# Optimization experiments

Measured on AMD Instinct MI355X. Metric: run time of the kernel, lower is better.

The kernel has to match this reference:

```python
import jax, jax.numpy as jnp
import numpy as np

N = 100_000      # nodes
E = 1_600_000    # edges (before self loops)
F_IN = 128       # dataset.num_node_features
H = 64           # hidden_channels
C = 10           # dataset.num_classes
B = 128          # graphs in batch
NEG_SLOPE = 0.2  # GATConv default


def setup_inputs() -> dict:
    key = jax.random.key(0)
    ks = jax.random.split(key, 16)
    s = 0.05
    x = jax.random.normal(ks[0], (N, F_IN), jnp.float32)
    edge_index = jax.random.randint(ks[1], (2, E), 0, N, dtype=jnp.int32).astype(jnp.int64)
    batch = jnp.sort(jax.random.randint(ks[2], (N,), 0, B, dtype=jnp.int32)).astype(jnp.int64)
    inp = {"x": x, "edge_index": edge_index, "batch": batch}
    # GATConv params: lin weight [out,in], att_src/att_dst [out], bias [out]
    dims = [(H, F_IN), (H, H), (H, H)]
    for i, (o, fi) in enumerate(dims, start=1):
        k = jax.random.split(ks[2 + i], 4)
        inp[f"W{i}"] = jax.random.normal(k[0], (o, fi), jnp.float32) * s
        inp[f"a_src{i}"] = jax.random.normal(k[1], (o,), jnp.float32) * s
        inp[f"a_dst{i}"] = jax.random.normal(k[2], (o,), jnp.float32) * s
        inp[f"b{i}"] = jax.random.normal(k[3], (o,), jnp.float32) * s
    inp["W_lin"] = jax.random.normal(ks[8], (C, H), jnp.float32) * s
    inp["b_lin"] = jax.random.normal(ks[9], (C,), jnp.float32) * s
    return inp


def gat_conv(x, src, dst, W, a_src, a_dst, b):
    # x: [N,Fin]; src/dst: [E+N] (self loops appended)
    h = x @ W.T                      # [N,H]
    e_src = h @ a_src                # [N] per-node src score
    e_dst = h @ a_dst                # [N] per-node dst score
    e = jax.nn.leaky_relu(e_src[src] + e_dst[dst], NEG_SLOPE)  # [E+N]
    # segment softmax over incoming edges of each dst node
    m = jax.ops.segment_max(e, dst, num_segments=N)
    ex = jnp.exp(e - m[dst])
    denom = jax.ops.segment_sum(ex, dst, num_segments=N)
    alpha = ex / denom[dst]          # [E+N]
    out = jax.ops.segment_sum(h[src] * alpha[:, None], dst, num_segments=N)
    return out + b


def reference(x, edge_index, batch, W1, a_src1, a_dst1, b1,
              W2, a_src2, a_dst2, b2, W3, a_src3, a_dst3, b3,
              W_lin, b_lin):
    loops = jnp.arange(N, dtype=edge_index.dtype)
    src = jnp.concatenate([edge_index[0], loops])
    dst = jnp.concatenate([edge_index[1], loops])
    h = jax.nn.relu(gat_conv(x, src, dst, W1, a_src1, a_dst1, b1))
    h = jax.nn.relu(gat_conv(h, src, dst, W2, a_src2, a_dst2, b2))
    h = gat_conv(h, src, dst, W3, a_src3, a_dst3, b3)
    # global mean pool over graphs
    sums = jax.ops.segment_sum(h, batch, num_segments=B)          # [B,H]
    cnt = jax.ops.segment_sum(jnp.ones((N,), h.dtype), batch, num_segments=B)
    pooled = sums / jnp.maximum(cnt, 1.0)[:, None]
    # dropout is identity in eval mode
    return pooled @ W_lin.T + b_lin   # [B,C]
```

## Files before the change

kernel.cpp:

```cpp
#include <hip/hip_runtime.h>
#include <hip/hip_bf16.h>

#define NN 100000
#define EE 1600000
#define ETOT 1700000
#define FIN1 128
#define HD 64
#define NC 10
#define NB 128
#define NEG 0.2f
#define LOG2E 1.44269504f

#define NBKT 196
#define BCAP 10240
#define BLKE 4096
#define ABLOCKS ((ETOT + BLKE - 1) / BLKE)
#define GBLOCKS ((NN + 63) / 64)


static constexpr size_t OFF_HA   = 0;
static constexpr size_t OFF_HB   = (size_t)NN * HD;
static constexpr size_t OFF_ESA  = (size_t)NN * HD * 2;
static constexpr size_t OFF_EDA  = OFF_ESA + (size_t)NN * 4;
static constexpr size_t OFF_ESB  = OFF_EDA + (size_t)NN * 4;
static constexpr size_t OFF_EDB  = OFF_ESB + (size_t)NN * 4;
static constexpr size_t OFF_ROW  = OFF_EDB + (size_t)NN * 4;
static constexpr size_t OFF_CSR  = OFF_ROW + (size_t)(NN + 4) * 4;
static constexpr size_t OFF_GC   = OFF_CSR + (size_t)ETOT * 4;
static constexpr size_t OFF_POOL = OFF_GC + 1024;
static constexpr size_t OFF_BKT  = OFF_POOL + (size_t)NB * HD * 4;

typedef __attribute__((ext_vector_type(8))) short short8;
typedef __attribute__((ext_vector_type(4))) float floatx4;
typedef __attribute__((ext_vector_type(2))) float floatx2;

__device__ __forceinline__ unsigned short f2bf(float f) {
  unsigned u = __float_as_uint(f);
  if ((u & 0x7F800000u) == 0x7F800000u) return (unsigned short)(u >> 16);
  return (unsigned short)((u + 0x7FFFu + ((u >> 16) & 1u)) >> 16);
}
__device__ __forceinline__ unsigned pk2(float a, float b) {
  return (unsigned)f2bf(a) | ((unsigned)f2bf(b) << 16);
}

#if __has_builtin(__builtin_amdgcn_cvt_pk_fp8_f32) && __has_builtin(__builtin_amdgcn_cvt_pk_f32_fp8)
#define HW_FP8 1
#endif
__device__ __forceinline__ unsigned enc1_fp8(float f) {
  _Float16 hf = (_Float16)f;
  unsigned short b = __builtin_bit_cast(unsigned short, hf);
  unsigned s = ((unsigned)b >> 8) & 0x80u;
  int mag = b & 0x7fff;
  if (mag < 0x2380) return s;
  int r = mag + 0x3F + ((mag >> 7) & 1);
  int m = (r >> 7) - 64;
  if (m > 0x7E) m = 0x7E;
  return s | (unsigned)m;
}
__device__ __forceinline__ unsigned pack4_fp8(float a, float b, float c, float d) {
#ifdef HW_FP8
  int w = __builtin_amdgcn_cvt_pk_fp8_f32(a, b, 0, false);
  w = __builtin_amdgcn_cvt_pk_fp8_f32(c, d, w, true);
  return (unsigned)w;
#else
  return enc1_fp8(a) | (enc1_fp8(b) << 8) | (enc1_fp8(c) << 16) | (enc1_fp8(d) << 24);
#endif
}
__device__ __forceinline__ float dec1_fp8(unsigned byte) {
  unsigned short hb = (unsigned short)(((byte & 0x80u) << 8) | ((byte & 0x7fu) << 7));
  _Float16 hf = __builtin_bit_cast(_Float16, hb);
  return (float)hf * 256.0f;
}
template <bool HI>
__device__ __forceinline__ floatx2 unpk2_fp8(unsigned w) {
#ifdef HW_FP8
  return __builtin_amdgcn_cvt_pk_f32_fp8((int)w, HI);
#else
  unsigned s = HI ? (w >> 16) : w;
  floatx2 r; r.x = dec1_fp8(s & 0xffu); r.y = dec1_fp8((s >> 8) & 0xffu);
  return r;
#endif
}

__device__ __forceinline__ void bucketA_body(
    int bid, const int* __restrict__ EI, unsigned* __restrict__ bucketed,
    int* __restrict__ gcur, char* smem) {
  unsigned* stage = (unsigned*)smem;
  unsigned short* sb = (unsigned short*)(smem + BLKE * 4);
  int* cnt  = (int*)(smem + BLKE * 4 + BLKE * 2);
  int* lofs = cnt + NBKT;
  int* base = lofs + NBKT;
  int* sc   = base + NBKT;
  const int t = threadIdx.x;
  const long long start = (long long)bid * BLKE;
  long long rem = (long long)ETOT - start;
  const int V = (rem < BLKE) ? (int)rem : BLKE;
  unsigned pk[BLKE / 256];
  short bk[BLKE / 256];
  for (int i = t; i < NBKT; i += 256) cnt[i] = 0;
  __syncthreads();
#pragma unroll
  for (int j = 0; j < BLKE / 256; j++) {
    long long k = start + t + 256 * j;
    bk[j] = -1;
    if (k < ETOT) {
      int s, d;
      if (k < EE) { s = EI[k]; d = EI[(long long)EE + k]; }
      else        { s = d = (int)(k - EE); }
      int b = d >> 9;
      pk[j] = ((unsigned)s << 9) | (unsigned)(d & 511);
      bk[j] = (short)b;
      atomicAdd(&cnt[b], 1);
    }
  }
  __syncthreads();
  int own = (t < NBKT) ? cnt[t] : 0;
  sc[t] = own;
  __syncthreads();
  for (int off = 1; off < 256; off <<= 1) {
    int add = (t >= off) ? sc[t - off] : 0;
    __syncthreads();
    sc[t] += add;
    __syncthreads();
  }
  if (t < NBKT) {
    lofs[t] = sc[t] - own;
    base[t] = (own > 0) ? atomicAdd(&gcur[t], own) : 0;
    cnt[t] = 0;
  }
  __syncthreads();
#pragma unroll
  for (int j = 0; j < BLKE / 256; j++) {
    if (bk[j] >= 0) {
      int b = bk[j];
      int p = lofs[b] + atomicAdd(&cnt[b], 1);
      stage[p] = pk[j];
      sb[p] = (unsigned short)b;
    }
  }
  __syncthreads();
  for (int i = t; i < V; i += 256) {
    int b = sb[i];
    int pos = base[b] + (i - lofs[b]);
    if (pos < BCAP) bucketed[(long long)b * BCAP + pos] = stage[i];
  }
}

__device__ __forceinline__ void gemm1_body(
    int bid, const float* __restrict__ X, const float* __restrict__ W,
    const float* __restrict__ As, const float* __restrict__ Ad,
    unsigned* __restrict__ hout, float* __restrict__ es, float* __restrict__ ed,
    char* smem) {
  constexpr int K = FIN1, RW = K / 2;
  unsigned* Xw = (unsigned*)smem;
  unsigned* Ww = (unsigned*)(smem + 16384);
  const int t = threadIdx.x;
  const int nodeBase = bid * 64;

  for (int i4 = t * 4; i4 < 64 * K; i4 += 1024) {
    int node = i4 >> 7, k = i4 & (K - 1);
    float4 v = make_float4(0.f, 0.f, 0.f, 0.f);
    if (nodeBase + node < NN)
      v = *(const float4*)(X + ((long long)(nodeBase + node) << 7) + k);
    uint2 p = make_uint2(pk2(v.x, v.y), pk2(v.z, v.w));
    int kw = k >> 1;
    *(uint2*)&Xw[node * RW + (kw ^ ((node & 7) << 2))] = p;
  }
  for (int i4 = t * 4; i4 < 64 * K; i4 += 1024) {
    int f = i4 >> 7, k = i4 & (K - 1);
    float4 v = *(const float4*)(W + ((long long)f << 7) + k);
    uint2 p = make_uint2(pk2(v.x, v.y), pk2(v.z, v.w));
    int kw = k >> 1;
    *(uint2*)&Ww[f * RW + (kw ^ ((f & 7) << 2))] = p;
  }
  __syncthreads();

  const int w = t >> 6, l = t & 63, m = l & 15, q = l >> 4;
  const int nodeLoc = 16 * w + m;
  const int sxa = (nodeLoc & 7) << 2;
  floatx4 acc[4];
#pragma unroll
  for (int nt = 0; nt < 4; nt++) acc[nt] = (floatx4){0.f, 0.f, 0.f, 0.f};
#pragma unroll
  for (int kc = 0; kc < K; kc += 32) {
    const int kcw = (kc >> 1) + 4 * q;
    short8 af = *(const short8*)&Xw[nodeLoc * RW + (kcw ^ sxa)];
#pragma unroll
    for (int nt = 0; nt < 4; nt++) {
      int f = 16 * nt + m;
      short8 bf = *(const short8*)&Ww[f * RW + (kcw ^ ((f & 7) << 2))];
      acc[nt] = __builtin_amdgcn_mfma_f32_16x16x32_bf16(af, bf, acc[nt], 0, 0, 0);
    }
  }
  float asv[4], adv[4];
#pragma unroll
  for (int nt = 0; nt < 4; nt++) { asv[nt] = As[16 * nt + m]; adv[nt] = Ad[16 * nt + m]; }
#pragma unroll
  for (int r = 0; r < 4; r++) {
    float ss = 0.f, sd2 = 0.f;
#pragma unroll
    for (int nt = 0; nt < 4; nt++) {
      ss = fmaf(acc[nt][r], asv[nt], ss);
      sd2 = fmaf(acc[nt][r], adv[nt], sd2);
    }
#pragma unroll
    for (int off = 1; off < 16; off <<= 1) {
      ss += __shfl_xor(ss, off);
      sd2 += __shfl_xor(sd2, off);
    }
    if (m == 0) {
      int gn = nodeBase + 16 * w + 4 * q + r;
      if (gn < NN) { es[gn] = ss * LOG2E; ed[gn] = sd2 * LOG2E; }
    }
  }
  {
    int gn = nodeBase + 16 * w + 4 * q;
#pragma unroll
    for (int nt = 0; nt < 4; nt++) {
#pragma unroll
      for (int r = 0; r < 4; r++) {
        float v = acc[nt][r];
        float p1 = __shfl_xor(v, 1);
        float p2 = __shfl_xor(v, 2);
        float p3 = __shfl_xor(v, 3);
        if ((m & 3) == 0 && (gn + r) < NN)
          hout[(gn + r) * 16 + 4 * nt + (m >> 2)] = pack4_fp8(v, p1, p2, p3);
      }
    }
  }
}

__global__ __launch_bounds__(256) void buildA_gemm1_kernel(
    const int* __restrict__ EI, unsigned* __restrict__ bucketed, int* __restrict__ gcur,
    const float* __restrict__ X, const float* __restrict__ W,
    const float* __restrict__ As, const float* __restrict__ Ad,
    unsigned* __restrict__ hout, float* __restrict__ es, float* __restrict__ ed) {
  __shared__ __align__(16) char smem[32768];
  if (blockIdx.x < ABLOCKS)
    bucketA_body(blockIdx.x, EI, bucketed, gcur, smem);
  else
    gemm1_body(blockIdx.x - ABLOCKS, X, W, As, Ad, hout, es, ed, smem);
}

__global__ __launch_bounds__(1024) void bucketB_kernel(
    const unsigned* __restrict__ bucketed, const int* __restrict__ gcur,
    int* __restrict__ rowptr, int* __restrict__ csr) {
  __shared__ int sc[256];
  __shared__ int hist[512];
  __shared__ int cur[512];
  __shared__ int ssum[256];
  const int t = threadIdx.x;
  const int b = blockIdx.x;
  if (t < 256) sc[t] = (t < NBKT) ? gcur[t] : 0;
  __syncthreads();
  for (int off = 1; off < 256; off <<= 1) {
    int add = (t >= off && t < 256) ? sc[t - off] : 0;
    __syncthreads();
    if (t < 256) sc[t] += add;
    __syncthreads();
  }
  const int cnt = gcur[b];
  const int base = sc[b] - cnt;
  if (b == 0 && t == 0) rowptr[NN] = ETOT;
  const unsigned* bp = bucketed + (long long)b * BCAP;
  if (t < 512) hist[t] = 0;
  __syncthreads();
  for (int i = t; i < cnt; i += 1024) atomicAdd(&hist[bp[i] & 511], 1);
  __syncthreads();
  int a0 = 0, a1 = 0, s = 0;
  if (t < 256) {
    a0 = hist[2 * t];
    a1 = hist[2 * t + 1];
    s = a0 + a1;
    ssum[t] = s;
  }
  __syncthreads();
  for (int off = 1; off < 256; off <<= 1) {
    int add = (t >= off && t < 256) ? ssum[t - off] : 0;
    __syncthreads();
    if (t < 256) ssum[t] += add;
    __syncthreads();
  }
  if (t < 256) {
    int ex = ssum[t] - s;
    cur[2 * t] = ex;
    cur[2 * t + 1] = ex + a0;
    int gn = b * 512 + 2 * t;
    if (gn < NN) rowptr[gn] = base + ex;
    if (gn + 1 < NN) rowptr[gn + 1] = base + ex + a0;
  }
  __syncthreads();
  for (int i = t; i < cnt; i += 1024) {
    unsigned e = bp[i];
    int pos = atomicAdd(&cur[e & 511], 1);
    csr[base + pos] = (int)(e >> 9);
  }
}

__global__ __launch_bounds__(256) void agg_gemm_kernel(
    const int* __restrict__ rowptr, const int* __restrict__ csr,
    const float* __restrict__ esIn, const float* __restrict__ edIn,
    const uint2* __restrict__ h8In, const float* __restrict__ biasA,
    const float* __restrict__ W, const float* __restrict__ As,
    const float* __restrict__ Ad,
    unsigned* __restrict__ hOut, float* __restrict__ esOut, float* __restrict__ edOut) {
  constexpr int K = HD, RW = K / 2;
  __shared__ unsigned Xw[64 * RW];
  __shared__ unsigned Ww[64 * RW];
  const int t = threadIdx.x;
  const int nodeBase = blockIdx.x * 64;

  for (int i4 = t * 4; i4 < 64 * K; i4 += 1024) {
    int f = i4 >> 6, k = i4 & (K - 1);
    float4 v = *(const float4*)(W + ((long long)f << 6) + k);
    uint2 p = make_uint2(pk2(v.x, v.y), pk2(v.z, v.w));
    int kw = k >> 1;
    *(uint2*)&Ww[f * RW + (kw ^ ((f & 7) << 2))] = p;
  }

  const int fl = t & 7;
#pragma unroll
  for (int half = 0; half < 2; half++) {
    const int nl = half * 32 + (t >> 3);
    const int n = nodeBase + nl;
    const int sxa = (nl & 7) << 2;
    const int kwb = (4 * fl) ^ sxa;
    if (n < NN) {
      const float edn = edIn[n];
      const int row = rowptr[n];
      const int end = rowptr[n + 1];
      const int endm1 = end - 1;
      float den = 0.f;
      float acc[8];
#pragma unroll
      for (int j = 0; j < 8; j++) acc[j] = 0.f;
      for (int i = row; i < end; i += 4) {
        int k1 = i + 1, k2 = i + 2, k3 = i + 3;
        k1 = (k1 < end) ? k1 : endm1;
        k2 = (k2 < end) ? k2 : endm1;
        k3 = (k3 < end) ? k3 : endm1;
        int s0 = csr[i], s1 = csr[k1], s2 = csr[k2], s3 = csr[k3];
        uint2 u0 = h8In[s0 * 8 + fl];
        uint2 u1 = h8In[s1 * 8 + fl];
        uint2 u2 = h8In[s2 * 8 + fl];
        uint2 u3 = h8In[s3 * 8 + fl];
        float e0 = esIn[s0] + edn, e1 = esIn[s1] + edn;
        float e2 = esIn[s2] + edn, e3 = esIn[s3] + edn;
        e0 = fmaxf(e0, NEG * e0);
        e1 = fmaxf(e1, NEG * e1);
        e2 = fmaxf(e2, NEG * e2);
        e3 = fmaxf(e3, NEG * e3);
        float w0 = exp2f(e0), w1 = exp2f(e1), w2 = exp2f(e2), w3 = exp2f(e3);
        w1 = (i + 1 < end) ? w1 : 0.f;
        w2 = (i + 2 < end) ? w2 : 0.f;
        w3 = (i + 3 < end) ? w3 : 0.f;
        den += (w0 + w1) + (w2 + w3);
#define ACC_E(w, u)                                            \
        { floatx2 fA = unpk2_fp8<false>((u).x);                \
          floatx2 fB = unpk2_fp8<true>((u).x);                 \
          floatx2 fC = unpk2_fp8<false>((u).y);                \
          floatx2 fD = unpk2_fp8<true>((u).y);                 \
          acc[0] = fmaf(w, fA.x, acc[0]); acc[1] = fmaf(w, fA.y, acc[1]); \
          acc[2] = fmaf(w, fB.x, acc[2]); acc[3] = fmaf(w, fB.y, acc[3]); \
          acc[4] = fmaf(w, fC.x, acc[4]); acc[5] = fmaf(w, fC.y, acc[5]); \
          acc[6] = fmaf(w, fD.x, acc[6]); acc[7] = fmaf(w, fD.y, acc[7]); }
        ACC_E(w0, u0) ACC_E(w1, u1) ACC_E(w2, u2) ACC_E(w3, u3)
#undef ACC_E
      }
      const float inv = 1.0f / den;
      float v[8];
#pragma unroll
      for (int j = 0; j < 8; j++)
        v[j] = fmaxf(acc[j] * inv + biasA[8 * fl + j], 0.f);
      *(uint2*)&Xw[nl * RW + kwb] = make_uint2(pk2(v[0], v[1]), pk2(v[2], v[3]));
      *(uint2*)&Xw[nl * RW + kwb + 2] = make_uint2(pk2(v[4], v[5]), pk2(v[6], v[7]));
    } else {
      *(uint2*)&Xw[nl * RW + kwb] = make_uint2(0u, 0u);
      *(uint2*)&Xw[nl * RW + kwb + 2] = make_uint2(0u, 0u);
    }
  }
  __syncthreads();

  const int w = t >> 6, l = t & 63, m = l & 15, q = l >> 4;
  const int nodeLoc = 16 * w + m;
  const int sxa = (nodeLoc & 7) << 2;
  floatx4 acc[4];
#pragma unroll
  for (int nt = 0; nt < 4; nt++) acc[nt] = (floatx4){0.f, 0.f, 0.f, 0.f};
#pragma unroll
  for (int kc = 0; kc < K; kc += 32) {
    const int kcw = (kc >> 1) + 4 * q;
    short8 af = *(const short8*)&Xw[nodeLoc * RW + (kcw ^ sxa)];
#pragma unroll
    for (int nt = 0; nt < 4; nt++) {
      int f = 16 * nt + m;
      short8 bf = *(const short8*)&Ww[f * RW + (kcw ^ ((f & 7) << 2))];
      acc[nt] = __builtin_amdgcn_mfma_f32_16x16x32_bf16(af, bf, acc[nt], 0, 0, 0);
    }
  }
  float asv[4], adv[4];
#pragma unroll
  for (int nt = 0; nt < 4; nt++) { asv[nt] = As[16 * nt + m]; adv[nt] = Ad[16 * nt + m]; }
#pragma unroll
  for (int r = 0; r < 4; r++) {
    float ss = 0.f, sd2 = 0.f;
#pragma unroll
    for (int nt = 0; nt < 4; nt++) {
      ss = fmaf(acc[nt][r], asv[nt], ss);
      sd2 = fmaf(acc[nt][r], adv[nt], sd2);
    }
#pragma unroll
    for (int off = 1; off < 16; off <<= 1) {
      ss += __shfl_xor(ss, off);
      sd2 += __shfl_xor(sd2, off);
    }
    if (m == 0) {
      int gn = nodeBase + 16 * w + 4 * q + r;
      if (gn < NN) { esOut[gn] = ss * LOG2E; edOut[gn] = sd2 * LOG2E; }
    }
  }
  {
    int gn = nodeBase + 16 * w + 4 * q;
#pragma unroll
    for (int nt = 0; nt < 4; nt++) {
#pragma unroll
      for (int r = 0; r < 4; r++) {
        float v = acc[nt][r];
        float p1 = __shfl_xor(v, 1);
        float p2 = __shfl_xor(v, 2);
        float p3 = __shfl_xor(v, 3);
        if ((m & 3) == 0 && (gn + r) < NN)
          hOut[(gn + r) * 16 + 4 * nt + (m >> 2)] = pack4_fp8(v, p1, p2, p3);
      }
    }
  }
}

__global__ __launch_bounds__(256) void agg3_pool_kernel(
    const int* __restrict__ rowptr, const int* __restrict__ csr,
    const float* __restrict__ esIn, const float* __restrict__ edIn,
    const uint2* __restrict__ h8In, const float* __restrict__ biasA,
    const int* __restrict__ batch, float* __restrict__ pooled) {
  __shared__ float P[32 * 66];
  __shared__ int gl[32];
  const int t = threadIdx.x;
  const int fl = t & 7;
  const int nl = t >> 3;
  const int n = blockIdx.x * 32 + nl;
  if (t < 32) gl[t] = batch[blockIdx.x * 32 + t];
  {
    const float edn = edIn[n];
    const int row = rowptr[n];
    const int end = rowptr[n + 1];
    const int endm1 = end - 1;
    float den = 0.f;
    float acc[8];
#pragma unroll
    for (int j = 0; j < 8; j++) acc[j] = 0.f;
    for (int i = row; i < end; i += 4) {
      int k1 = i + 1, k2 = i + 2, k3 = i + 3;
      k1 = (k1 < end) ? k1 : endm1;
      k2 = (k2 < end) ? k2 : endm1;
      k3 = (k3 < end) ? k3 : endm1;
      int s0 = csr[i], s1 = csr[k1], s2 = csr[k2], s3 = csr[k3];
      uint2 u0 = h8In[s0 * 8 + fl];
      uint2 u1 = h8In[s1 * 8 + fl];
      uint2 u2 = h8In[s2 * 8 + fl];
      uint2 u3 = h8In[s3 * 8 + fl];
      float e0 = esIn[s0] + edn, e1 = esIn[s1] + edn;
      float e2 = esIn[s2] + edn, e3 = esIn[s3] + edn;
      e0 = fmaxf(e0, NEG * e0);
      e1 = fmaxf(e1, NEG * e1);
      e2 = fmaxf(e2, NEG * e2);
      e3 = fmaxf(e3, NEG * e3);
      float w0 = exp2f(e0), w1 = exp2f(e1), w2 = exp2f(e2), w3 = exp2f(e3);
      w1 = (i + 1 < end) ? w1 : 0.f;
      w2 = (i + 2 < end) ? w2 : 0.f;
      w3 = (i + 3 < end) ? w3 : 0.f;
      den += (w0 + w1) + (w2 + w3);
#define ACC_E(w, u)                                            \
      { floatx2 fA = unpk2_fp8<false>((u).x);                  \
        floatx2 fB = unpk2_fp8<true>((u).x);                   \
        floatx2 fC = unpk2_fp8<false>((u).y);                  \
        floatx2 fD = unpk2_fp8<true>((u).y);                   \
        acc[0] = fmaf(w, fA.x, acc[0]); acc[1] = fmaf(w, fA.y, acc[1]); \
        acc[2] = fmaf(w, fB.x, acc[2]); acc[3] = fmaf(w, fB.y, acc[3]); \
        acc[4] = fmaf(w, fC.x, acc[4]); acc[5] = fmaf(w, fC.y, acc[5]); \
        acc[6] = fmaf(w, fD.x, acc[6]); acc[7] = fmaf(w, fD.y, acc[7]); }
      ACC_E(w0, u0) ACC_E(w1, u1) ACC_E(w2, u2) ACC_E(w3, u3)
#undef ACC_E
    }
    const float inv = 1.0f / den;
#pragma unroll
    for (int j = 0; j < 8; j++)
      P[nl * 66 + 8 * fl + j] = acc[j] * inv + biasA[8 * fl + j];
  }
  __syncthreads();
  if (t < HD) {
    const int f = t;
    float s = 0.f;
    int gcur = gl[0];
    for (int k = 0; k < 32; k++) {
      int g = gl[k];
      if (g != gcur) {
        atomicAdd(&pooled[gcur * HD + f], s);
        s = 0.f;
        gcur = g;
      }
      s += P[k * 66 + f];
    }
    atomicAdd(&pooled[gcur * HD + f], s);
  }
}

__device__ __forceinline__ int lower_bound_batch(const int* bt, int target) {
  int lo = 0, hi = NN;
  while (lo < hi) {
    int mid = (lo + hi) >> 1;
    if (bt[mid] < target) lo = mid + 1; else hi = mid;
  }
  return lo;
}

__global__ void final_kernel(
    const float* __restrict__ pooled, const int* __restrict__ batch,
    const float* __restrict__ Wlin, const float* __restrict__ blin,
    float* __restrict__ out) {
  int t = blockIdx.x * blockDim.x + threadIdx.x;
  if (t >= NB * NC) return;
  int b = t / NC, c = t - b * NC;
  int lo = lower_bound_batch(batch, b);
  int hi = lower_bound_batch(batch, b + 1);
  float inv = 1.0f / fmaxf((float)(hi - lo), 1.0f);
  float a = blin[c];
#pragma unroll 16
  for (int f = 0; f < HD; f++)
    a = fmaf(pooled[b * HD + f] * inv, Wlin[(long long)c * HD + f], a);
  out[t] = a;
}

extern "C" void kernel_launch(void* const* d_in, const int* in_sizes, int n_in,
                              void* d_out, int out_size, void* d_ws, size_t ws_size,
                              hipStream_t stream) {
  char* ws = (char*)d_ws;
  unsigned* hA       = (unsigned*)(ws + OFF_HA);
  unsigned* hB       = (unsigned*)(ws + OFF_HB);
  float*    esA      = (float*)(ws + OFF_ESA);
  float*    edA      = (float*)(ws + OFF_EDA);
  float*    esB      = (float*)(ws + OFF_ESB);
  float*    edB      = (float*)(ws + OFF_EDB);
  int*      rowptr   = (int*)(ws + OFF_ROW);
  int*      csr      = (int*)(ws + OFF_CSR);
  int*      gcur     = (int*)(ws + OFF_GC);
  float*    pooled   = (float*)(ws + OFF_POOL);
  unsigned* bucketed = (unsigned*)(ws + OFF_BKT);

  const float* X  = (const float*)d_in[0];
  const int*   EI = (const int*)d_in[1];
  const int*   BT = (const int*)d_in[2];
  const float* Wm[3] = {(const float*)d_in[3], (const float*)d_in[7], (const float*)d_in[11]};
  const float* As[3] = {(const float*)d_in[4], (const float*)d_in[8], (const float*)d_in[12]};
  const float* Ad[3] = {(const float*)d_in[5], (const float*)d_in[9], (const float*)d_in[13]};
  const float* Bb[3] = {(const float*)d_in[6], (const float*)d_in[10], (const float*)d_in[14]};
  const float* Wl = (const float*)d_in[15];
  const float* bl = (const float*)d_in[16];

  (void)hipMemsetAsync(gcur, 0, 1024 + (size_t)NB * HD * 4, stream);
  buildA_gemm1_kernel<<<ABLOCKS + GBLOCKS, 256, 0, stream>>>(
      EI, bucketed, gcur, X, Wm[0], As[0], Ad[0], hA, esA, edA);
  bucketB_kernel<<<NBKT, 1024, 0, stream>>>(bucketed, gcur, rowptr, csr);
  agg_gemm_kernel<<<GBLOCKS, 256, 0, stream>>>(
      rowptr, csr, esA, edA, (const uint2*)hA, Bb[0],
      Wm[1], As[1], Ad[1], hB, esB, edB);
  agg_gemm_kernel<<<GBLOCKS, 256, 0, stream>>>(
      rowptr, csr, esB, edB, (const uint2*)hB, Bb[1],
      Wm[2], As[2], Ad[2], hA, esA, edA);
  agg3_pool_kernel<<<NN / 32, 256, 0, stream>>>(
      rowptr, csr, esA, edA, (const uint2*)hA, Bb[2], BT, pooled);
  final_kernel<<<(NB * NC + 255) / 256, 256, 0, stream>>>(pooled, BT, Wl, bl, (float*)d_out);
}
```

Before: 281.6 us.

## Aggregate with 4 lanes per node, 16B fp8 gathers and shuffled edge scores

Reworks the per-node aggregation so each node is handled by 4 lanes, each owning 16 features and loading them with one 16-byte gather, instead of 8 lanes with 8-byte gathers. Each lane now loads a single csr index and source score per group of four edges and shares them across the quad with shuffles, with the next group's index and score prefetched. The pooling kernel is changed to process 64 nodes per block to match. This is meant to cut redundant csr and score loads and raise bytes per gather, at the cost of more accumulator registers, shuffle overhead and less parallelism per node.

```diff
diff --git a/kernel.cpp b/kernel.cpp
--- a/kernel.cpp
+++ b/kernel.cpp
@@ -80,6 +80,68 @@
   floatx2 r; r.x = dec1_fp8(s & 0xffu); r.y = dec1_fp8((s >> 8) & 0xffu);
   return r;
 #endif
+}
+
+__device__ __forceinline__ void acc16(float* acc, float w, uint4 u) {
+  floatx2 f0 = unpk2_fp8<false>(u.x), f1 = unpk2_fp8<true>(u.x);
+  floatx2 f2 = unpk2_fp8<false>(u.y), f3 = unpk2_fp8<true>(u.y);
+  floatx2 f4 = unpk2_fp8<false>(u.z), f5 = unpk2_fp8<true>(u.z);
+  floatx2 f6 = unpk2_fp8<false>(u.w), f7 = unpk2_fp8<true>(u.w);
+  acc[0]  = fmaf(w, f0.x, acc[0]);  acc[1]  = fmaf(w, f0.y, acc[1]);
+  acc[2]  = fmaf(w, f1.x, acc[2]);  acc[3]  = fmaf(w, f1.y, acc[3]);
+  acc[4]  = fmaf(w, f2.x, acc[4]);  acc[5]  = fmaf(w, f2.y, acc[5]);
+  acc[6]  = fmaf(w, f3.x, acc[6]);  acc[7]  = fmaf(w, f3.y, acc[7]);
+  acc[8]  = fmaf(w, f4.x, acc[8]);  acc[9]  = fmaf(w, f4.y, acc[9]);
+  acc[10] = fmaf(w, f5.x, acc[10]); acc[11] = fmaf(w, f5.y, acc[11]);
+  acc[12] = fmaf(w, f6.x, acc[12]); acc[13] = fmaf(w, f6.y, acc[13]);
+  acc[14] = fmaf(w, f7.x, acc[14]); acc[15] = fmaf(w, f7.y, acc[15]);
+}
+
+__device__ __forceinline__ float aggregate_node(
+    int n, int fl, const int* __restrict__ rowptr, const int* __restrict__ csr,
+    const float* __restrict__ esIn, const float* __restrict__ edIn,
+    const uint4* __restrict__ h16, float* acc) {
+#pragma unroll
+  for (int j = 0; j < 16; j++) acc[j] = 0.f;
+  const float edn = edIn[n];
+  const int row = rowptr[n];
+  const int end = rowptr[n + 1];
+  const int endm1 = end - 1;
+  float den = 0.f;
+  int idx0 = row + fl;
+  int s_cur = csr[(idx0 < end) ? idx0 : endm1];
+  float ev_cur = esIn[s_cur];
+  for (int i = row; i < end; i += 4) {
+    int inext = i + 4;
+    int s_nxt = s_cur;
+    if (inext < end) {
+      int idn = inext + fl;
+      s_nxt = csr[(idn < end) ? idn : endm1];
+    }
+    float ev_nxt = esIn[s_nxt];
+    float e = ev_cur + edn;
+    e = fmaxf(e, NEG * e);
+    float w = exp2f(e);
+    w = (i + fl < end) ? w : 0.f;
+    den += w;
+    int s0 = __shfl(s_cur, 0, 4), s1 = __shfl(s_cur, 1, 4);
+    int s2 = __shfl(s_cur, 2, 4), s3 = __shfl(s_cur, 3, 4);
+    float w0 = __shfl(w, 0, 4), w1 = __shfl(w, 1, 4);
+    float w2 = __shfl(w, 2, 4), w3 = __shfl(w, 3, 4);
+    uint4 u0 = h16[s0 * 4 + fl];
+    uint4 u1 = h16[s1 * 4 + fl];
+    uint4 u2 = h16[s2 * 4 + fl];
+    uint4 u3 = h16[s3 * 4 + fl];
+    acc16(acc, w0, u0);
+    acc16(acc, w1, u1);
+    acc16(acc, w2, u2);
+    acc16(acc, w3, u3);
+    s_cur = s_nxt;
+    ev_cur = ev_nxt;
+  }
+  den += __shfl_xor(den, 1, 4);
+  den += __shfl_xor(den, 2, 4);
+  return 1.0f / den;
 }
 
 __device__ __forceinline__ void bucketA_body(
@@ -300,7 +362,7 @@
 __global__ __launch_bounds__(256) void agg_gemm_kernel(
     const int* __restrict__ rowptr, const int* __restrict__ csr,
     const float* __restrict__ esIn, const float* __restrict__ edIn,
-    const uint2* __restrict__ h8In, const float* __restrict__ biasA,
+    const uint4* __restrict__ h16In, const float* __restrict__ biasA,
     const float* __restrict__ W, const float* __restrict__ As,
     const float* __restrict__ Ad,
     unsigned* __restrict__ hOut, float* __restrict__ esOut, float* __restrict__ edOut) {
@@ -318,79 +380,42 @@
     *(uint2*)&Ww[f * RW + (kw ^ ((f & 7) << 2))] = p;
   }
 
-  const int fl = t & 7;
-#pragma unroll
-  for (int half = 0; half < 2; half++) {
-    const int nl = half * 32 + (t >> 3);
-    const int n = nodeBase + nl;
-    const int sxa = (nl & 7) << 2;
-    const int kwb = (4 * fl) ^ sxa;
-    if (n < NN) {
-      const float edn = edIn[n];
-      const int row = rowptr[n];
-      const int end = rowptr[n + 1];
-      const int endm1 = end - 1;
-      float den = 0.f;
-      float acc[8];
-#pragma unroll
-      for (int j = 0; j < 8; j++) acc[j] = 0.f;
-      for (int i = row; i < end; i += 4) {
-        int k1 = i + 1, k2 = i + 2, k3 = i + 3;
-        k1 = (k1 < end) ? k1 : endm1;
-        k2 = (k2 < end) ? k2 : endm1;
-        k3 = (k3 < end) ? k3 : endm1;
-        int s0 = csr[i], s1 = csr[k1], s2 = csr[k2], s3 = csr[k3];
-        uint2 u0 = h8In[s0 * 8 + fl];
-        uint2 u1 = h8In[s1 * 8 + fl];
-        uint2 u2 = h8In[s2 * 8 + fl];
-        uint2 u3 = h8In[s3 * 8 + fl];
-        float e0 = esIn[s0] + edn, e1 = esIn[s1] + edn;
-        float e2 = esIn[s2] + edn, e3 = esIn[s3] + edn;
-        e0 = fmaxf(e0, NEG * e0);
-        e1 = fmaxf(e1, NEG * e1);
-        e2 = fmaxf(e2, NEG * e2);
-        e3 = fmaxf(e3, NEG * e3);
-        float w0 = exp2f(e0), w1 = exp2f(e1), w2 = exp2f(e2), w3 = exp2f(e3);
-        w1 = (i + 1 < end) ? w1 : 0.f;
-        w2 = (i + 2 < end) ? w2 : 0.f;
-        w3 = (i + 3 < end) ? w3 : 0.f;
-        den += (w0 + w1) + (w2 + w3);
-#define ACC_E(w, u)                                            \
-        { floatx2 fA = unpk2_fp8<false>((u).x);                \
-          floatx2 fB = unpk2_fp8<true>((u).x);                 \
-          floatx2 fC = unpk2_fp8<false>((u).y);                \
-          floatx2 fD = unpk2_fp8<true>((u).y);                 \
-          acc[0] = fmaf(w, fA.x, acc[0]); acc[1] = fmaf(w, fA.y, acc[1]); \
-          acc[2] = fmaf(w, fB.x, acc[2]); acc[3] = fmaf(w, fB.y, acc[3]); \
-          acc[4] = fmaf(w, fC.x, acc[4]); acc[5] = fmaf(w, fC.y, acc[5]); \
-          acc[6] = fmaf(w, fD.x, acc[6]); acc[7] = fmaf(w, fD.y, acc[7]); }
-        ACC_E(w0, u0) ACC_E(w1, u1) ACC_E(w2, u2) ACC_E(w3, u3)
-#undef ACC_E
-      }
-      const float inv = 1.0f / den;
-      float v[8];
-#pragma unroll
-      for (int j = 0; j < 8; j++)
-        v[j] = fmaxf(acc[j] * inv + biasA[8 * fl + j], 0.f);
-      *(uint2*)&Xw[nl * RW + kwb] = make_uint2(pk2(v[0], v[1]), pk2(v[2], v[3]));
-      *(uint2*)&Xw[nl * RW + kwb + 2] = make_uint2(pk2(v[4], v[5]), pk2(v[6], v[7]));
-    } else {
-      *(uint2*)&Xw[nl * RW + kwb] = make_uint2(0u, 0u);
-      *(uint2*)&Xw[nl * RW + kwb + 2] = make_uint2(0u, 0u);
-    }
+  const int fl = t & 3;
+  const int nl = t >> 2;
+  const int n = nodeBase + nl;
+  const int sxa = (nl & 7) << 2;
+  const int wb0 = nl * RW + ((fl * 8) ^ sxa);
+  const int wb1 = nl * RW + ((fl * 8 + 4) ^ sxa);
+  if (n < NN) {
+    float acc[16];
+    const float inv = aggregate_node(n, fl, rowptr, csr, esIn, edIn, h16In, acc);
+    float v[16];
+#pragma unroll
+    for (int j = 0; j < 16; j++)
+      v[j] = fmaxf(acc[j] * inv + biasA[16 * fl + j], 0.f);
+    uint4 pa, pb;
+    pa.x = pk2(v[0], v[1]);   pa.y = pk2(v[2], v[3]);
+    pa.z = pk2(v[4], v[5]);   pa.w = pk2(v[6], v[7]);
+    pb.x = pk2(v[8], v[9]);   pb.y = pk2(v[10], v[11]);
+    pb.z = pk2(v[12], v[13]); pb.w = pk2(v[14], v[15]);
+    *(uint4*)&Xw[wb0] = pa;
+    *(uint4*)&Xw[wb1] = pb;
+  } else {
+    *(uint4*)&Xw[wb0] = make_uint4(0u, 0u, 0u, 0u);
+    *(uint4*)&Xw[wb1] = make_uint4(0u, 0u, 0u, 0u);
   }
   __syncthreads();
 
   const int w = t >> 6, l = t & 63, m = l & 15, q = l >> 4;
   const int nodeLoc = 16 * w + m;
-  const int sxa = (nodeLoc & 7) << 2;
+  const int sxb = (nodeLoc & 7) << 2;
   floatx4 acc[4];
 #pragma unroll
   for (int nt = 0; nt < 4; nt++) acc[nt] = (floatx4){0.f, 0.f, 0.f, 0.f};
 #pragma unroll
   for (int kc = 0; kc < K; kc += 32) {
     const int kcw = (kc >> 1) + 4 * q;
-    short8 af = *(const short8*)&Xw[nodeLoc * RW + (kcw ^ sxa)];
+    short8 af = *(const short8*)&Xw[nodeLoc * RW + (kcw ^ sxb)];
 #pragma unroll
     for (int nt = 0; nt < 4; nt++) {
       int f = 16 * nt + m;
@@ -439,68 +464,35 @@
 __global__ __launch_bounds__(256) void agg3_pool_kernel(
     const int* __restrict__ rowptr, const int* __restrict__ csr,
     const float* __restrict__ esIn, const float* __restrict__ edIn,
-    const uint2* __restrict__ h8In, const float* __restrict__ biasA,
+    const uint4* __restrict__ h16In, const float* __restrict__ biasA,
     const int* __restrict__ batch, float* __restrict__ pooled) {
-  __shared__ float P[32 * 66];
-  __shared__ int gl[32];
+  __shared__ float P[64 * 66];
+  __shared__ int gl[64];
   const int t = threadIdx.x;
-  const int fl = t & 7;
-  const int nl = t >> 3;
-  const int n = blockIdx.x * 32 + nl;
-  if (t < 32) gl[t] = batch[blockIdx.x * 32 + t];
-  {
-    const float edn = edIn[n];
-    const int row = rowptr[n];
-    const int end = rowptr[n + 1];
-    const int endm1 = end - 1;
-    float den = 0.f;
-    float acc[8];
-#pragma unroll
-    for (int j = 0; j < 8; j++) acc[j] = 0.f;
-    for (int i = row; i < end; i += 4) {
-      int k1 = i + 1, k2 = i + 2, k3 = i + 3;
-      k1 = (k1 < end) ? k1 : endm1;
-      k2 = (k2 < end) ? k2 : endm1;
-      k3 = (k3 < end) ? k3 : endm1;
-      int s0 = csr[i], s1 = csr[k1], s2 = csr[k2], s3 = csr[k3];
-      uint2 u0 = h8In[s0 * 8 + fl];
-      uint2 u1 = h8In[s1 * 8 + fl];
-      uint2 u2 = h8In[s2 * 8 + fl];
-      uint2 u3 = h8In[s3 * 8 + fl];
-      float e0 = esIn[s0] + edn, e1 = esIn[s1] + edn;
-      float e2 = esIn[s2] + edn, e3 = esIn[s3] + edn;
-      e0 = fmaxf(e0, NEG * e0);
-      e1 = fmaxf(e1, NEG * e1);
-      e2 = fmaxf(e2, NEG * e2);
-      e3 = fmaxf(e3, NEG * e3);
-      float w0 = exp2f(e0), w1 = exp2f(e1), w2 = exp2f(e2), w3 = exp2f(e3);
-      w1 = (i + 1 < end) ? w1 : 0.f;
-      w2 = (i + 2 < end) ? w2 : 0.f;
-      w3 = (i + 3 < end) ? w3 : 0.f;
-      den += (w0 + w1) + (w2 + w3);
-#define ACC_E(w, u)                                            \
-      { floatx2 fA = unpk2_fp8<false>((u).x);                  \
-        floatx2 fB = unpk2_fp8<true>((u).x);                   \
-        floatx2 fC = unpk2_fp8<false>((u).y);                  \
-        floatx2 fD = unpk2_fp8<true>((u).y);                   \
-        acc[0] = fmaf(w, fA.x, acc[0]); acc[1] = fmaf(w, fA.y, acc[1]); \
-        acc[2] = fmaf(w, fB.x, acc[2]); acc[3] = fmaf(w, fB.y, acc[3]); \
-        acc[4] = fmaf(w, fC.x, acc[4]); acc[5] = fmaf(w, fC.y, acc[5]); \
-        acc[6] = fmaf(w, fD.x, acc[6]); acc[7] = fmaf(w, fD.y, acc[7]); }
-      ACC_E(w0, u0) ACC_E(w1, u1) ACC_E(w2, u2) ACC_E(w3, u3)
-#undef ACC_E
-    }
-    const float inv = 1.0f / den;
-#pragma unroll
-    for (int j = 0; j < 8; j++)
-      P[nl * 66 + 8 * fl + j] = acc[j] * inv + biasA[8 * fl + j];
+  const int fl = t & 3;
+  const int nl = t >> 2;
+  const int n = blockIdx.x * 64 + nl;
+  if (t < 64) {
+    int bn = blockIdx.x * 64 + t;
+    gl[t] = batch[(bn < NN) ? bn : (NN - 1)];
+  }
+  if (n < NN) {
+    float acc[16];
+    const float inv = aggregate_node(n, fl, rowptr, csr, esIn, edIn, h16In, acc);
+#pragma unroll
+    for (int j = 0; j < 16; j++)
+      P[nl * 66 + 16 * fl + j] = acc[j] * inv + biasA[16 * fl + j];
+  } else {
+#pragma unroll
+    for (int j = 0; j < 16; j++)
+      P[nl * 66 + 16 * fl + j] = 0.f;
   }
   __syncthreads();
   if (t < HD) {
     const int f = t;
     float s = 0.f;
     int gcur = gl[0];
-    for (int k = 0; k < 32; k++) {
+    for (int k = 0; k < 64; k++) {
       int g = gl[k];
       if (g != gcur) {
         atomicAdd(&pooled[gcur * HD + f], s);
@@ -570,12 +562,12 @@
       EI, bucketed, gcur, X, Wm[0], As[0], Ad[0], hA, esA, edA);
   bucketB_kernel<<<NBKT, 1024, 0, stream>>>(bucketed, gcur, rowptr, csr);
   agg_gemm_kernel<<<GBLOCKS, 256, 0, stream>>>(
-      rowptr, csr, esA, edA, (const uint2*)hA, Bb[0],
+      rowptr, csr, esA, edA, (const uint4*)hA, Bb[0],
       Wm[1], As[1], Ad[1], hB, esB, edB);
   agg_gemm_kernel<<<GBLOCKS, 256, 0, stream>>>(
-      rowptr, csr, esB, edB, (const uint2*)hB, Bb[1],
+      rowptr, csr, esB, edB, (const uint4*)hB, Bb[1],
       Wm[2], As[2], Ad[2], hA, esA, edA);
-  agg3_pool_kernel<<<NN / 32, 256, 0, stream>>>(
-      rowptr, csr, esA, edA, (const uint2*)hA, Bb[2], BT, pooled);
+  agg3_pool_kernel<<<GBLOCKS, 256, 0, stream>>>(
+      rowptr, csr, esA, edA, (const uint4*)hA, Bb[2], BT, pooled);
   final_kernel<<<(NB * NC + 255) / 256, 256, 0, stream>>>(pooled, BT, Wl, bl, (float*)d_out);
 }
```

Result: no change. 286.3 us (+1.7%).
